# Kernel tuning notes

Measured on AMD Instinct MI355X. Metric: run time of the kernel, lower is better.

The kernel has to match this reference:

```python
import jax, jax.numpy as jnp
import numpy as np

B, L, D, H = 1, 512, 64, 64
EPS = 1e-5


def _ln(x, w, b):
    mu = jnp.mean(x, axis=-1, keepdims=True)
    var = jnp.var(x, axis=-1, keepdims=True)
    return (x - mu) * jax.lax.rsqrt(var + EPS) * w + b


def setup_inputs() -> dict:
    key = jax.random.key(0)
    ks = jax.random.split(key, 16)
    s = 0.02
    return {
        "x": jax.random.normal(ks[0], (B, L, L, D), dtype=jnp.float32),
        "sequence_mask": jax.random.randint(ks[1], (B, L), 0, 2, dtype=jnp.int32),
        "norm_w": jnp.ones((D,), jnp.float32),
        "norm_b": jnp.zeros((D,), jnp.float32),
        "left_w": jax.random.normal(ks[2], (D, H), jnp.float32) * s,
        "left_b": jnp.zeros((H,), jnp.float32),
        "right_w": jax.random.normal(ks[3], (D, H), jnp.float32) * s,
        "right_b": jnp.zeros((H,), jnp.float32),
        "lgate_w": jax.random.normal(ks[4], (D, H), jnp.float32) * s,
        "lgate_b": jnp.ones((H,), jnp.float32),
        "rgate_w": jax.random.normal(ks[5], (D, H), jnp.float32) * s,
        "rgate_b": jnp.ones((H,), jnp.float32),
        "ogate_w": jax.random.normal(ks[6], (D, D), jnp.float32) * s,
        "ogate_b": jnp.ones((D,), jnp.float32),
        "onorm_w": jnp.ones((H,), jnp.float32),
        "onorm_b": jnp.zeros((H,), jnp.float32),
        "out_w": jax.random.normal(ks[7], (H, D), jnp.float32) * s,
        "out_b": jnp.zeros((D,), jnp.float32),
    }


def reference(x, sequence_mask, norm_w, norm_b, left_w, left_b, right_w, right_b,
              lgate_w, lgate_b, rgate_w, rgate_b, ogate_w, ogate_b,
              onorm_w, onorm_b, out_w, out_b):
    xn = _ln(x, norm_w, norm_b)                              # (B,L,L,D)
    left = xn @ left_w + left_b                              # (B,L,L,H)
    right = xn @ right_w + right_b
    m = sequence_mask.astype(xn.dtype)                       # (B,L)
    mask = (m[:, :, None] * m[:, None, :])[..., None]        # (B,L,L,1)
    left = left * mask
    right = right * mask
    left = left * jax.nn.sigmoid(xn @ lgate_w + lgate_b)
    right = right * jax.nn.sigmoid(xn @ rgate_w + rgate_b)
    out_gate = jax.nn.sigmoid(xn @ ogate_w + ogate_b)        # (B,L,L,D)
    # ingoing mix: out[i,j,d] = sum_k left[k,j,d] * right[k,i,d]
    out = jnp.einsum('bkjd,bkid->bijd', left, right)         # (B,L,L,H)
    out = _ln(out, onorm_w, onorm_b)
    out = out @ out_w + out_b                                # (B,L,L,D)
    return out * out_gate
```

## Files before the change

### kernel.cpp

```cpp
#include <hip/hip_runtime.h>


typedef __attribute__((ext_vector_type(4))) float f32x4;
typedef __attribute__((ext_vector_type(8))) __bf16 bf16x8;

__device__ __forceinline__ unsigned short f2bf(float f) {
  unsigned u = __float_as_uint(f);
  u += 0x7FFFu + ((u >> 16) & 1u);
  return (unsigned short)(u >> 16);
}
__device__ __forceinline__ float bf2f(unsigned short h) {
  return __uint_as_float(((unsigned)h) << 16);
}
__device__ __forceinline__ unsigned pk2bf(float a, float b) {
  unsigned short ua = __builtin_bit_cast(unsigned short, (__bf16)a);
  unsigned short ub = __builtin_bit_cast(unsigned short, (__bf16)b);
  return (unsigned)ua | ((unsigned)ub << 16);
}
__device__ __forceinline__ float sigm(float x) { return 1.0f / (1.0f + __expf(-x)); }

__global__ __launch_bounds__(256) void k0_prep(
    const float* __restrict__ lw, const float* __restrict__ rw,
    const float* __restrict__ lgw, const float* __restrict__ rgw,
    const float* __restrict__ ogw, unsigned short* __restrict__ wt) {
  const int t = threadIdx.x;
  #pragma unroll
  for (int e = 0; e < 80; ++e) {
    int idx = e * 256 + t;
    int n = idx >> 6, k = idx & 63;
    const float* W = (n < 64) ? lw : (n < 128) ? rw : (n < 192) ? lgw
                     : (n < 256) ? rgw : ogw;
    float v = W[k * 64 + (n & 63)];
    int el = n * 64 + ((((k >> 3) ^ (n & 7)) << 3) | (k & 7));
    wt[el] = f2bf(v);
  }
}

__global__ __launch_bounds__(512) void k1_proj(
    const float* __restrict__ x, const int* __restrict__ smask,
    const float* __restrict__ norm_w, const float* __restrict__ norm_b,
    const float* __restrict__ left_b, const float* __restrict__ right_b,
    const float* __restrict__ lgate_b, const float* __restrict__ rgate_b,
    const float* __restrict__ ogate_b, const unsigned short* __restrict__ wt,
    unsigned short* __restrict__ left_t, unsigned short* __restrict__ right_t,
    unsigned short* __restrict__ ogate) {
  __shared__ __align__(16) char ldsWt[40960];
  __shared__ __align__(16) char ldsX[16384];
  __shared__ float sNW[64], sNB[64];
  __shared__ __align__(16) float sLB[64], sRB[64], sLGB[64], sRGB[64], sOGB[64];
  __shared__ float sMK[128];

  const int t = threadIdx.x;
  const int c = blockIdx.x & 511;
  const int r0 = (blockIdx.x >> 9) << 7;

  #pragma unroll
  for (int i = 0; i < 5; ++i) {
    int u = t + i * 512;
    *(uint4*)(ldsWt + u * 16) = *(const uint4*)((const char*)wt + u * 16);
  }
  if (t < 64) {
    sNW[t] = norm_w[t]; sNB[t] = norm_b[t];
    sLB[t] = left_b[t]; sRB[t] = right_b[t];
    sLGB[t] = lgate_b[t]; sRGB[t] = rgate_b[t]; sOGB[t] = ogate_b[t];
  }
  if (t >= 64 && t < 192) sMK[t - 64] = (float)smask[r0 + (t - 64)];
  __syncthreads();

  {
    const int m = t >> 2, q = t & 3;
    const float* xp = x + ((size_t)(r0 + m) * 512 + c) * 64 + q * 16;
    float v[16];
    #pragma unroll
    for (int i = 0; i < 4; ++i) {
      float4 f = *(const float4*)(xp + i * 4);
      v[i*4+0] = f.x; v[i*4+1] = f.y; v[i*4+2] = f.z; v[i*4+3] = f.w;
    }
    float s = 0.f, ss = 0.f;
    #pragma unroll
    for (int i = 0; i < 16; ++i) { s += v[i]; ss += v[i] * v[i]; }
    s += __shfl_xor(s, 1); s += __shfl_xor(s, 2);
    ss += __shfl_xor(ss, 1); ss += __shfl_xor(ss, 2);
    const float mu = s * 0.015625f;
    const float rs = rsqrtf(ss * 0.015625f - mu * mu + 1e-5f);
    unsigned pk[8];
    #pragma unroll
    for (int i = 0; i < 8; ++i) {
      const int d0 = q * 16 + 2 * i;
      pk[i] = pk2bf((v[2*i]   - mu) * rs * sNW[d0]     + sNB[d0],
                    (v[2*i+1] - mu) * rs * sNW[d0 + 1] + sNB[d0 + 1]);
    }
    uint4 lo; lo.x = pk[0]; lo.y = pk[1]; lo.z = pk[2]; lo.w = pk[3];
    uint4 hi; hi.x = pk[4]; hi.y = pk[5]; hi.z = pk[6]; hi.w = pk[7];
    *(uint4*)(ldsX + m * 128 + (((q * 2)     ^ (m & 7)) << 4)) = lo;
    *(uint4*)(ldsX + m * 128 + (((q * 2 + 1) ^ (m & 7)) << 4)) = hi;
  }
  __syncthreads();

  const int w = t >> 6, l = t & 63, lr = l & 15, g = l >> 4;
  f32x4 acc[20];
  #pragma unroll
  for (int nf = 0; nf < 20; ++nf) acc[nf] = (f32x4){0.f, 0.f, 0.f, 0.f};
  const int rowA = w * 16 + lr;
  #pragma unroll
  for (int s = 0; s < 2; ++s) {
    const int soff = (((s * 4 + g) ^ (lr & 7)) << 4);
    bf16x8 a = *(const bf16x8*)(ldsX + rowA * 128 + soff);
    #pragma unroll
    for (int nf = 0; nf < 16; ++nf) {
      bf16x8 bb = *(const bf16x8*)(ldsWt + (nf * 16 + lr) * 128 + soff);
      acc[nf] = __builtin_amdgcn_mfma_f32_16x16x32_bf16(a, bb, acc[nf], 0, 0, 0);
    }
    #pragma unroll
    for (int nf = 16; nf < 20; ++nf) {
      bf16x8 bb = *(const bf16x8*)(ldsWt + (nf * 16 + lr) * 128 + soff);
      acc[nf] = __builtin_amdgcn_mfma_f32_16x16x32_bf16(bb, a, acc[nf], 0, 0, 0);
    }
  }
  __syncthreads();

  char* bL = ldsWt;
  char* bR = ldsWt + 17408;
  {
    const float mc = (float)smask[c];
    float mk[4];
    #pragma unroll
    for (int rr = 0; rr < 4; ++rr) mk[rr] = mc * sMK[w * 16 + g * 4 + rr];
    const int rb2 = (w * 16 + g * 4) * 2;
    #pragma unroll
    for (int nf = 0; nf < 4; ++nf) {
      const int hh = nf * 16 + lr;
      const float lb = sLB[hh], rb = sRB[hh];
      const float lgb = sLGB[hh], rgb = sRGB[hh];
      float lo[4], ro[4];
      #pragma unroll
      for (int rr = 0; rr < 4; ++rr) {
        lo[rr] = (acc[nf][rr]     + lb) * mk[rr] * sigm(acc[8  + nf][rr] + lgb);
        ro[rr] = (acc[4 + nf][rr] + rb) * mk[rr] * sigm(acc[12 + nf][rr] + rgb);
      }
      uint2 lv; lv.x = pk2bf(lo[0], lo[1]); lv.y = pk2bf(lo[2], lo[3]);
      uint2 rv; rv.x = pk2bf(ro[0], ro[1]); rv.y = pk2bf(ro[2], ro[3]);
      *(uint2*)(bL + hh * 272 + rb2) = lv;
      *(uint2*)(bR + hh * 272 + rb2) = rv;
    }
    const int rloc = w * 16 + lr;
    #pragma unroll
    for (int nf = 0; nf < 4; ++nf) {
      const int d0 = nf * 16 + g * 4;
      const float4 ob4 = *(const float4*)&sOGB[d0];
      const float g0 = sigm(acc[16 + nf][0] + ob4.x);
      const float g1 = sigm(acc[16 + nf][1] + ob4.y);
      const float g2 = sigm(acc[16 + nf][2] + ob4.z);
      const float g3 = sigm(acc[16 + nf][3] + ob4.w);
      uint2 gv; gv.x = pk2bf(g0, g1); gv.y = pk2bf(g2, g3);
      const int slot = (d0 >> 3) ^ (rloc & 7);
      *(uint2*)(ldsX + rloc * 128 + slot * 16 + (d0 & 4) * 2) = gv;
    }
  }
  __syncthreads();

  const int cx = c & 7;
  #pragma unroll
  for (int it = 0; it < 2; ++it) {
    const int idx = it * 512 + t;
    const int hh = idx >> 4, rel = idx & 15;
    const size_t goff = (size_t)hh * 524288 + (size_t)c * 1024 +
                        (size_t)(((r0 >> 3) + (rel & 8) + ((rel & 7) ^ cx)) << 4);
    *(uint4*)((char*)left_t  + goff) = *(const uint4*)(bL + hh * 272 + rel * 16);
    *(uint4*)((char*)right_t + goff) = *(const uint4*)(bR + hh * 272 + rel * 16);
  }
  #pragma unroll
  for (int it = 0; it < 2; ++it) {
    const int idx = it * 512 + t;
    const int rl = idx >> 3, ch = idx & 7;
    *(uint4*)((char*)ogate + ((size_t)(r0 + rl) * 512 + c) * 128 + ch * 16) =
        *(const uint4*)(ldsX + rl * 128 + ((ch ^ (rl & 7)) << 4));
  }
}

__global__ __launch_bounds__(512) void k2_einsum(
    const unsigned short* __restrict__ left_t,
    const unsigned short* __restrict__ right_t,
    unsigned short* __restrict__ o) {
  __shared__ __align__(16) char ldsA[32768];
  __shared__ __align__(16) char ldsB[32768];
  const int t = threadIdx.x;
  const int d = blockIdx.x >> 2;
  const int i0 = ((blockIdx.x >> 1) & 1) * 256;
  const int j0 = (blockIdx.x & 1) * 256;
  const int w = t >> 6, l = t & 63, lr = l & 15, g = l >> 4;
  const char* Rb = (const char*)right_t + (size_t)d * 524288;
  const char* Lb = (const char*)left_t  + (size_t)d * 524288;
  f32x4 acc[8][4];
  #pragma unroll
  for (int mi = 0; mi < 8; ++mi)
    #pragma unroll
    for (int nj = 0; nj < 4; ++nj) acc[mi][nj] = (f32x4){0.f, 0.f, 0.f, 0.f};
  const int wm0 = (w >> 2) * 128, wn0 = (w & 3) * 64;
  for (int kb = 0; kb < 512; kb += 64) {
    #pragma unroll
    for (int cc = 0; cc < 4; ++cc) {
      const int p16 = (w * 4 + cc) * 64 + l;
      const int m = p16 >> 3, sl = p16 & 7;
      *(uint4*)(ldsA + p16 * 16) =
          *(const uint4*)(Rb + (size_t)(i0 + m) * 1024 + kb * 2 + sl * 16);
      *(uint4*)(ldsB + p16 * 16) =
          *(const uint4*)(Lb + (size_t)(j0 + m) * 1024 + kb * 2 + sl * 16);
    }
    __syncthreads();
    #pragma unroll
    for (int s = 0; s < 2; ++s) {
      const int soff = (((s * 4 + g) ^ (lr & 7)) << 4);
      bf16x8 af[8], bfr[4];
      #pragma unroll
      for (int mi = 0; mi < 8; ++mi)
        af[mi] = *(const bf16x8*)(ldsA + (wm0 + mi * 16 + lr) * 128 + soff);
      #pragma unroll
      for (int nj = 0; nj < 4; ++nj)
        bfr[nj] = *(const bf16x8*)(ldsB + (wn0 + nj * 16 + lr) * 128 + soff);
      #pragma unroll
      for (int mi = 0; mi < 8; ++mi)
        #pragma unroll
        for (int nj = 0; nj < 4; ++nj)
          acc[mi][nj] = __builtin_amdgcn_mfma_f32_16x16x32_bf16(
              af[mi], bfr[nj], acc[mi][nj], 0, 0, 0);
    }
    __syncthreads();
  }
  #pragma unroll
  for (int mi = 0; mi < 8; ++mi)
    #pragma unroll
    for (int nj = 0; nj < 4; ++nj)
      #pragma unroll
      for (int rr = 0; rr < 4; ++rr) {
        const int i = i0 + wm0 + mi * 16 + g * 4 + rr;
        const int j = j0 + wn0 + nj * 16 + lr;
        o[(size_t)d * 262144 + (size_t)i * 512 + j] = f2bf(acc[mi][nj][rr]);
      }
}

__global__ __launch_bounds__(256) void k3_final(
    const unsigned short* __restrict__ o, const unsigned short* __restrict__ ogate,
    const float* __restrict__ onorm_w, const float* __restrict__ onorm_b,
    const float* __restrict__ out_w, const float* __restrict__ out_b,
    float* __restrict__ out) {
  __shared__ __align__(16) char ldsO[64 * 272];
  __shared__ __align__(16) float ldsW[64 * 68];
  __shared__ float sONW[64], sONB[64], sOB[64];
  const int t = threadIdx.x;
  const int i = blockIdx.x >> 2;
  const int j0 = (blockIdx.x & 3) << 7;
  const size_t p0 = (size_t)i * 512 + j0;

  #pragma unroll
  for (int e = 0; e < 4; ++e) {
    const int u = t + e * 256;
    const int d = u >> 4, sl = u & 15;
    *(uint4*)(ldsO + d * 272 + sl * 16) =
        *(const uint4*)((const char*)o + ((size_t)d * 262144 + p0) * 2 + sl * 16);
  }
  #pragma unroll
  for (int e = 0; e < 16; ++e) {
    const int idx = e * 256 + t;
    ldsW[(idx >> 6) * 68 + (idx & 63)] = out_w[idx];
  }
  if (t < 64) { sONW[t] = onorm_w[t]; sONB[t] = onorm_b[t]; sOB[t] = out_b[t]; }
  __syncthreads();

  const int p = t >> 1, h = t & 1;
  float v[32];
  #pragma unroll
  for (int dl = 0; dl < 32; ++dl)
    v[dl] = bf2f(*(const unsigned short*)(ldsO + (h * 32 + dl) * 272 + p * 2));
  float s = 0.f, ss = 0.f;
  #pragma unroll
  for (int dl = 0; dl < 32; ++dl) { s += v[dl]; ss += v[dl] * v[dl]; }
  s += __shfl_xor(s, 1); ss += __shfl_xor(ss, 1);
  const float mu = s * 0.015625f;
  const float rs = rsqrtf(ss * 0.015625f - mu * mu + 1e-5f);
  float xv[32];
  #pragma unroll
  for (int dl = 0; dl < 32; ++dl) {
    const int d = h * 32 + dl;
    xv[dl] = (v[dl] - mu) * rs * sONW[d] + sONB[d];
  }

  const int n0 = h * 32;
  float acc[32];
  #pragma unroll
  for (int n = 0; n < 32; ++n) acc[n] = 0.f;
  #pragma unroll 4
  for (int kk = 0; kk < 32; ++kk) {
    const float a = xv[kk];
    const float* wr = ldsW + (h * 32 + kk) * 68 + n0;
    #pragma unroll
    for (int c = 0; c < 8; ++c) {
      const float4 wv = *(const float4*)(wr + c * 4);
      acc[c*4+0] += a * wv.x; acc[c*4+1] += a * wv.y;
      acc[c*4+2] += a * wv.z; acc[c*4+3] += a * wv.w;
    }
  }
  #pragma unroll 4
  for (int kk = 0; kk < 32; ++kk) {
    const float a = __shfl_xor(xv[kk], 1);
    const float* wr = ldsW + ((1 - h) * 32 + kk) * 68 + n0;
    #pragma unroll
    for (int c = 0; c < 8; ++c) {
      const float4 wv = *(const float4*)(wr + c * 4);
      acc[c*4+0] += a * wv.x; acc[c*4+1] += a * wv.y;
      acc[c*4+2] += a * wv.z; acc[c*4+3] += a * wv.w;
    }
  }

  const size_t pl = p0 + p;
  const unsigned short* gp = ogate + pl * 64 + n0;
  float* op = out + pl * 64 + n0;
  #pragma unroll
  for (int c = 0; c < 4; ++c) {
    const uint4 g4 = *(const uint4*)(gp + c * 8);
    const unsigned gg[4] = {g4.x, g4.y, g4.z, g4.w};
    float r[8];
    #pragma unroll
    for (int e = 0; e < 4; ++e) {
      r[2*e]   = (acc[c*8 + 2*e]   + sOB[n0 + c*8 + 2*e])   *
                 bf2f((unsigned short)(gg[e] & 0xffffu));
      r[2*e+1] = (acc[c*8 + 2*e+1] + sOB[n0 + c*8 + 2*e+1]) *
                 bf2f((unsigned short)(gg[e] >> 16));
    }
    float4 s0; s0.x = r[0]; s0.y = r[1]; s0.z = r[2]; s0.w = r[3];
    float4 s1; s1.x = r[4]; s1.y = r[5]; s1.z = r[6]; s1.w = r[7];
    *(float4*)(op + c * 8)     = s0;
    *(float4*)(op + c * 8 + 4) = s1;
  }
}

extern "C" void kernel_launch(void* const* d_in, const int* in_sizes, int n_in,
                              void* d_out, int out_size, void* d_ws, size_t ws_size,
                              hipStream_t stream) {
  const float* x       = (const float*)d_in[0];
  const int*   sm      = (const int*)d_in[1];
  const float* norm_w  = (const float*)d_in[2];
  const float* norm_b  = (const float*)d_in[3];
  const float* left_w  = (const float*)d_in[4];
  const float* left_b  = (const float*)d_in[5];
  const float* right_w = (const float*)d_in[6];
  const float* right_b = (const float*)d_in[7];
  const float* lgate_w = (const float*)d_in[8];
  const float* lgate_b = (const float*)d_in[9];
  const float* rgate_w = (const float*)d_in[10];
  const float* rgate_b = (const float*)d_in[11];
  const float* ogate_w = (const float*)d_in[12];
  const float* ogate_b = (const float*)d_in[13];
  const float* onorm_w = (const float*)d_in[14];
  const float* onorm_b = (const float*)d_in[15];
  const float* out_w   = (const float*)d_in[16];
  const float* out_b   = (const float*)d_in[17];

  char* ws = (char*)d_ws;
  unsigned short* left_t  = (unsigned short*)(ws + 0);
  unsigned short* right_t = (unsigned short*)(ws + 33554432);
  unsigned short* ogate   = (unsigned short*)(ws + 67108864);
  unsigned short* obuf    = (unsigned short*)(ws + 100663296);
  unsigned short* wt      = (unsigned short*)(ws + 134217728);

  if (ws_size < (size_t)134217728 + 40960) return;

  k0_prep<<<dim3(1), dim3(256), 0, stream>>>(left_w, right_w, lgate_w, rgate_w,
                                             ogate_w, wt);
  k1_proj<<<dim3(2048), dim3(512), 0, stream>>>(x, sm, norm_w, norm_b, left_b,
                                                right_b, lgate_b, rgate_b,
                                                ogate_b, wt, left_t, right_t,
                                                ogate);
  k2_einsum<<<dim3(256), dim3(512), 0, stream>>>(left_t, right_t, obuf);
  k3_final<<<dim3(2048), dim3(256), 0, stream>>>(obuf, ogate, onorm_w, onorm_b,
                                                 out_w, out_b, (float*)d_out);
}
```

Baseline: 140.4 us.

## Stage einsum output through LDS, use direct global-to-LDS loads, parallelize weight prep

```diff
diff --git a/kernel.cpp b/kernel.cpp
--- a/kernel.cpp
+++ b/kernel.cpp
@@ -23,10 +23,10 @@
     const float* __restrict__ lw, const float* __restrict__ rw,
     const float* __restrict__ lgw, const float* __restrict__ rgw,
     const float* __restrict__ ogw, unsigned short* __restrict__ wt) {
-  const int t = threadIdx.x;
-  #pragma unroll
-  for (int e = 0; e < 80; ++e) {
-    int idx = e * 256 + t;
+  const int t0 = blockIdx.x * 1024 + threadIdx.x;
+  #pragma unroll
+  for (int e = 0; e < 4; ++e) {
+    int idx = t0 + e * 256;
     int n = idx >> 6, k = idx & 63;
     const float* W = (n < 64) ? lw : (n < 128) ? rw : (n < 192) ? lgw
                      : (n < 256) ? rgw : ogw;
@@ -182,12 +182,15 @@
     const unsigned short* __restrict__ left_t,
     const unsigned short* __restrict__ right_t,
     unsigned short* __restrict__ o) {
-  __shared__ __align__(16) char ldsA[32768];
-  __shared__ __align__(16) char ldsB[32768];
+  __shared__ __align__(16) char lds[69632];
+  char* ldsA = lds;
+  char* ldsB = lds + 32768;
   const int t = threadIdx.x;
-  const int d = blockIdx.x >> 2;
-  const int i0 = ((blockIdx.x >> 1) & 1) * 256;
-  const int j0 = (blockIdx.x & 1) * 256;
+  const int bid = (int)blockIdx.x;
+  const int id = ((bid & 7) << 5) | (bid >> 3);
+  const int d = id >> 2;
+  const int i0 = ((id >> 1) & 1) * 256;
+  const int j0 = (id & 1) * 256;
   const int w = t >> 6, l = t & 63, lr = l & 15, g = l >> 4;
   const char* Rb = (const char*)right_t + (size_t)d * 524288;
   const char* Lb = (const char*)left_t  + (size_t)d * 524288;
@@ -202,10 +205,12 @@
     for (int cc = 0; cc < 4; ++cc) {
       const int p16 = (w * 4 + cc) * 64 + l;
       const int m = p16 >> 3, sl = p16 & 7;
-      *(uint4*)(ldsA + p16 * 16) =
-          *(const uint4*)(Rb + (size_t)(i0 + m) * 1024 + kb * 2 + sl * 16);
-      *(uint4*)(ldsB + p16 * 16) =
-          *(const uint4*)(Lb + (size_t)(j0 + m) * 1024 + kb * 2 + sl * 16);
+      __builtin_amdgcn_global_load_lds(
+          (const void*)(Rb + (size_t)(i0 + m) * 1024 + kb * 2 + sl * 16),
+          (void*)(ldsA + p16 * 16), 16, 0, 0);
+      __builtin_amdgcn_global_load_lds(
+          (const void*)(Lb + (size_t)(j0 + m) * 1024 + kb * 2 + sl * 16),
+          (void*)(ldsB + p16 * 16), 16, 0, 0);
     }
     __syncthreads();
     #pragma unroll
@@ -228,15 +233,30 @@
     __syncthreads();
   }
   #pragma unroll
-  for (int mi = 0; mi < 8; ++mi)
-    #pragma unroll
-    for (int nj = 0; nj < 4; ++nj)
-      #pragma unroll
-      for (int rr = 0; rr < 4; ++rr) {
-        const int i = i0 + wm0 + mi * 16 + g * 4 + rr;
-        const int j = j0 + wn0 + nj * 16 + lr;
-        o[(size_t)d * 262144 + (size_t)i * 512 + j] = f2bf(acc[mi][nj][rr]);
-      }
+  for (int h2 = 0; h2 < 2; ++h2) {
+    if ((w >> 2) == h2) {
+      #pragma unroll
+      for (int mi = 0; mi < 8; ++mi)
+        #pragma unroll
+        for (int nj = 0; nj < 4; ++nj)
+          #pragma unroll
+          for (int rr = 0; rr < 4; ++rr) {
+            const int rl = mi * 16 + g * 4 + rr;
+            const int col = wn0 + nj * 16 + lr;
+            *(unsigned short*)(lds + rl * 544 + col * 2) = f2bf(acc[mi][nj][rr]);
+          }
+    }
+    __syncthreads();
+    #pragma unroll
+    for (int it = 0; it < 8; ++it) {
+      const int q = it * 512 + t;
+      const int rl = q >> 5, ch = q & 31;
+      *(uint4*)((char*)o + (size_t)d * 524288 +
+                (size_t)(i0 + h2 * 128 + rl) * 1024 + (size_t)j0 * 2 + ch * 16) =
+          *(const uint4*)(lds + rl * 544 + ch * 16);
+    }
+    __syncthreads();
+  }
 }
 
 __global__ __launch_bounds__(256) void k3_final(
@@ -365,8 +385,8 @@
 
   if (ws_size < (size_t)134217728 + 40960) return;
 
-  k0_prep<<<dim3(1), dim3(256), 0, stream>>>(left_w, right_w, lgate_w, rgate_w,
-                                             ogate_w, wt);
+  k0_prep<<<dim3(20), dim3(256), 0, stream>>>(left_w, right_w, lgate_w, rgate_w,
+                                              ogate_w, wt);
   k1_proj<<<dim3(2048), dim3(512), 0, stream>>>(x, sm, norm_w, norm_b, left_b,
                                                 right_b, lgate_b, rgate_b,
                                                 ogate_b, wt, left_t, right_t,
```

Result: faster. 129.0 us (-8.1%).
